# Kernel tuning notes

Measured on AMD Instinct MI355X. Metric: run time of the kernel, lower is better.

The kernel has to match this reference:

```python
import jax, jax.numpy as jnp
import numpy as np

N, A, B, C = 256, 1024, 64, 16


def setup_inputs() -> dict:
    key = jax.random.key(0)
    k1, k2, k3 = jax.random.split(key, 3)
    x = jax.random.normal(k1, (N, A), dtype=jnp.float32)
    weight = jax.random.normal(k2, (A, B * C), dtype=jnp.float32) * 0.02
    bias = jax.random.normal(k3, (B,), dtype=jnp.float32) * 0.02
    return {"x": x, "weight": weight, "bias": bias}


def reference(x, weight, bias):
    # x: [N, A]; weight: [A, B*C]; bias: [B]
    n = x.shape[0]
    mat = (x @ weight).reshape(n, B, C)              # [N, B, C]
    # pairwise L1 over the C (kernel) axis -> [N, N, B]
    l1 = jnp.abs(mat[:, None, :, :] - mat[None, :, :, :]).sum(axis=-1)
    # exp(-L1), sum over the first (broadcast) axis as in the torch code,
    # which includes the self term exp(0)=1
    out = jnp.exp(-l1).sum(axis=0) + bias            # [N, B]
    return out
```

## Files before the change

kernel.cpp:

```cpp
#include <hip/hip_runtime.h>

#define LOG2E 1.4426950408889634f

typedef __bf16 bf16x8 __attribute__((ext_vector_type(8)));
typedef float  f32x4  __attribute__((ext_vector_type(4)));

__device__ inline unsigned short f2bf(float f){
  unsigned u = __float_as_uint(f);
  unsigned r = u + 0x7FFFu + ((u >> 16) & 1u);
  return (unsigned short)(r >> 16);
}
__device__ inline unsigned pack2(float lo, float hi){
  return (unsigned)f2bf(lo) | ((unsigned)f2bf(hi) << 16);
}

__global__ __launch_bounds__(256) void k_gemm_ks(const float* __restrict__ X,
                                                 const float* __restrict__ Wm,
                                                 float* __restrict__ P){
  __shared__ unsigned short As[64 * 72];
  __shared__ unsigned short Bs[64 * 72];
  const int m0 = blockIdx.x * 64, n0 = blockIdx.y * 64;
  const int k0 = blockIdx.z * 256;
  const int t = threadIdx.x;
  const int lane = t & 63, w = t >> 6;
  const int wrow = (w & 1) * 32, wcol = (w >> 1) * 32;
  const int r16 = lane & 15, quad = lane >> 4;

  const int ar = t >> 2, aq = t & 3;
  const int bc = t & 15, bg = t >> 4;
  const float* ap = X + (size_t)(m0 + ar) * 1024 + k0 + aq * 16;
  const float* bp = Wm + (size_t)k0 * 1024 + n0 + bc * 4;

  f32x4 acc[2][2];
  #pragma unroll
  for (int p = 0; p < 2; ++p)
    #pragma unroll
    for (int q = 0; q < 2; ++q)
      #pragma unroll
      for (int e = 0; e < 4; ++e) acc[p][q][e] = 0.f;

  float4 pa[4], pb[4];
  #pragma unroll
  for (int r = 0; r < 4; ++r) pa[r] = *(const float4*)(ap + r * 4);
  #pragma unroll
  for (int r = 0; r < 4; ++r) pb[r] = *(const float4*)(bp + (size_t)(4 * bg + r) * 1024);

  #pragma unroll
  for (int kt = 0; kt < 256; kt += 64){
    __syncthreads();
    {
      unsigned short* d = &As[ar * 72 + aq * 16];
      uint4 o;
      o.x = pack2(pa[0].x, pa[0].y); o.y = pack2(pa[0].z, pa[0].w);
      o.z = pack2(pa[1].x, pa[1].y); o.w = pack2(pa[1].z, pa[1].w);
      *(uint4*)d = o;
      o.x = pack2(pa[2].x, pa[2].y); o.y = pack2(pa[2].z, pa[2].w);
      o.z = pack2(pa[3].x, pa[3].y); o.w = pack2(pa[3].z, pa[3].w);
      *(uint4*)(d + 8) = o;
    }
    {
      #pragma unroll
      for (int e = 0; e < 4; ++e){
        const int n = bc * 4 + e;
        uint2 o;
        o.x = pack2(((const float*)&pb[0])[e], ((const float*)&pb[1])[e]);
        o.y = pack2(((const float*)&pb[2])[e], ((const float*)&pb[3])[e]);
        const int cw = (bg >> 1) ^ ((n >> 3) & 7);
        *(uint2*)(&Bs[n * 72 + cw * 8 + (bg & 1) * 4]) = o;
      }
    }
    __syncthreads();
    if (kt < 192){
      #pragma unroll
      for (int r = 0; r < 4; ++r) pa[r] = *(const float4*)(ap + kt + 64 + r * 4);
      #pragma unroll
      for (int r = 0; r < 4; ++r) pb[r] = *(const float4*)(bp + (size_t)(kt + 64 + 4 * bg + r) * 1024);
    }
    #pragma unroll
    for (int kk = 0; kk < 2; ++kk){
      const int ko = kk * 32 + quad * 8;
      bf16x8 a0 = *(const bf16x8*)(&As[(wrow      + r16) * 72 + ko]);
      bf16x8 a1 = *(const bf16x8*)(&As[(wrow + 16 + r16) * 72 + ko]);
      const int c = kk * 4 + quad;
      const int nb0 = wcol + r16, nb1 = wcol + 16 + r16;
      bf16x8 b0 = *(const bf16x8*)(&Bs[nb0 * 72 + ((c ^ ((nb0 >> 3) & 7)) * 8)]);
      bf16x8 b1 = *(const bf16x8*)(&Bs[nb1 * 72 + ((c ^ ((nb1 >> 3) & 7)) * 8)]);
      acc[0][0] = __builtin_amdgcn_mfma_f32_16x16x32_bf16(a0, b0, acc[0][0], 0, 0, 0);
      acc[0][1] = __builtin_amdgcn_mfma_f32_16x16x32_bf16(a0, b1, acc[0][1], 0, 0, 0);
      acc[1][0] = __builtin_amdgcn_mfma_f32_16x16x32_bf16(a1, b0, acc[1][0], 0, 0, 0);
      acc[1][1] = __builtin_amdgcn_mfma_f32_16x16x32_bf16(a1, b1, acc[1][1], 0, 0, 0);
    }
  }
  float* Pz = P + (size_t)blockIdx.z * 64 * 256 * 16;
  #pragma unroll
  for (int p = 0; p < 2; ++p)
    #pragma unroll
    for (int q = 0; q < 2; ++q)
      #pragma unroll
      for (int r = 0; r < 4; ++r){
        const int row = m0 + wrow + p * 16 + quad * 4 + r;
        const int col = n0 + wcol + q * 16 + r16;
        Pz[(size_t)(col >> 4) * 4096 + row * 16 + (col & 15)] = acc[p][q][r];
      }
}

__global__ __launch_bounds__(1024) void k_pair(const float* __restrict__ P,
                                               const float* __restrict__ bias,
                                               float* __restrict__ out){
  __shared__ float L[256 * 20];
  __shared__ float red[16][64];
  const int b = blockIdx.x >> 2, jc = blockIdx.x & 3;
  const int t = threadIdx.x, lane = t & 63, w = t >> 6;

  {
    const int i = t >> 2, q = t & 3;
    const float* base = P + (size_t)b * 4096 + t * 4;
    float4 s0 = *(const float4*)(base);
    float4 s1 = *(const float4*)(base + 262144);
    float4 s2 = *(const float4*)(base + 524288);
    float4 s3 = *(const float4*)(base + 786432);
    float4 r;
    r.x = (s0.x + s1.x) + (s2.x + s3.x);
    r.y = (s0.y + s1.y) + (s2.y + s3.y);
    r.z = (s0.z + s1.z) + (s2.z + s3.z);
    r.w = (s0.w + s1.w) + (s2.w + s3.w);
    *(float4*)(&L[i * 20 + q * 4]) = r;
  }
  __syncthreads();

  const int j = jc * 64 + lane;
  float oj[16];
  #pragma unroll
  for (int q = 0; q < 4; ++q){
    float4 v = *(const float4*)(&L[j * 20 + q * 4]);
    oj[q*4+0] = v.x; oj[q*4+1] = v.y; oj[q*4+2] = v.z; oj[q*4+3] = v.w;
  }

  float acc = 0.f;
  const int i0 = w * 16;
  #pragma unroll 4
  for (int ii = i0; ii < i0 + 16; ++ii){
    const float4* fr = (const float4*)(&L[ii * 20]);
    float4 f0 = fr[0], f1 = fr[1], f2 = fr[2], f3 = fr[3];
    float p0 = fabsf(oj[0]  - f0.x) + fabsf(oj[1]  - f0.y)
             + fabsf(oj[2]  - f0.z) + fabsf(oj[3]  - f0.w);
    float p1 = fabsf(oj[4]  - f1.x) + fabsf(oj[5]  - f1.y)
             + fabsf(oj[6]  - f1.z) + fabsf(oj[7]  - f1.w);
    float p2 = fabsf(oj[8]  - f2.x) + fabsf(oj[9]  - f2.y)
             + fabsf(oj[10] - f2.z) + fabsf(oj[11] - f2.w);
    float p3 = fabsf(oj[12] - f3.x) + fabsf(oj[13] - f3.y)
             + fabsf(oj[14] - f3.z) + fabsf(oj[15] - f3.w);
    acc += exp2f(-LOG2E * ((p0 + p1) + (p2 + p3)));
  }
  red[w][lane] = acc;
  __syncthreads();
  if (w == 0){
    float tot = 0.f;
    #pragma unroll
    for (int ww = 0; ww < 16; ++ww) tot += red[ww][lane];
    out[(size_t)j * 64 + b] = tot + bias[b];
  }
}

extern "C" void kernel_launch(void* const* d_in, const int* in_sizes, int n_in,
                              void* d_out, int out_size, void* d_ws, size_t ws_size,
                              hipStream_t stream){
  const float* x    = (const float*)d_in[0];
  const float* W    = (const float*)d_in[1];
  const float* bias = (const float*)d_in[2];
  float* out = (float*)d_out;
  float* P   = (float*)d_ws;

  k_gemm_ks<<<dim3(4, 16, 4), 256, 0, stream>>>(x, W, P);
  k_pair<<<256, 1024, 0, stream>>>(P, bias, out);
}
```

Measured before the change: 74.12 us.

## Widen GEMM blocks to 1024 threads, loading all K-chunks at once

The split-K GEMM now runs 1024 threads per block. Four thread groups each stage one 64-wide K chunk into separate LDS buffers with a single barrier, replacing the serial 4-step K loop with its register prefetch. Each wave now computes one 16x16 output tile over all chunks instead of a 32x32 tile, using two accumulators. The bf16 conversion switches to the HIP intrinsic. The aim is more memory parallelism and fewer barriers in a latency-bound small GEMM, at the cost of 4x LDS per block and less reuse per wave.

Result: no change. 74.08 us (-0.1%).

```diff
diff --git a/kernel.cpp b/kernel.cpp
--- a/kernel.cpp
+++ b/kernel.cpp
@@ -1,43 +1,33 @@
 #include <hip/hip_runtime.h>
+#include <hip/hip_bf16.h>
 
 #define LOG2E 1.4426950408889634f
 
 typedef __bf16 bf16x8 __attribute__((ext_vector_type(8)));
 typedef float  f32x4  __attribute__((ext_vector_type(4)));
 
-__device__ inline unsigned short f2bf(float f){
-  unsigned u = __float_as_uint(f);
-  unsigned r = u + 0x7FFFu + ((u >> 16) & 1u);
-  return (unsigned short)(r >> 16);
-}
 __device__ inline unsigned pack2(float lo, float hi){
-  return (unsigned)f2bf(lo) | ((unsigned)f2bf(hi) << 16);
+  __hip_bfloat162 h = __float22bfloat162_rn(make_float2(lo, hi));
+  return *reinterpret_cast<unsigned*>(&h);
 }
 
-__global__ __launch_bounds__(256) void k_gemm_ks(const float* __restrict__ X,
-                                                 const float* __restrict__ Wm,
-                                                 float* __restrict__ P){
-  __shared__ unsigned short As[64 * 72];
-  __shared__ unsigned short Bs[64 * 72];
+__global__ __launch_bounds__(1024) void k_gemm_ks(const float* __restrict__ X,
+                                                  const float* __restrict__ Wm,
+                                                  float* __restrict__ P){
+  __shared__ unsigned short As[4][64 * 72];
+  __shared__ unsigned short Bs[4][64 * 72];
   const int m0 = blockIdx.x * 64, n0 = blockIdx.y * 64;
   const int k0 = blockIdx.z * 256;
   const int t = threadIdx.x;
   const int lane = t & 63, w = t >> 6;
-  const int wrow = (w & 1) * 32, wcol = (w >> 1) * 32;
+  const int g = t >> 8, s = t & 255;
   const int r16 = lane & 15, quad = lane >> 4;
+  const int wrow = (w & 3) * 16, wcol = (w >> 2) * 16;
 
-  const int ar = t >> 2, aq = t & 3;
-  const int bc = t & 15, bg = t >> 4;
-  const float* ap = X + (size_t)(m0 + ar) * 1024 + k0 + aq * 16;
-  const float* bp = Wm + (size_t)k0 * 1024 + n0 + bc * 4;
-
-  f32x4 acc[2][2];
-  #pragma unroll
-  for (int p = 0; p < 2; ++p)
-    #pragma unroll
-    for (int q = 0; q < 2; ++q)
-      #pragma unroll
-      for (int e = 0; e < 4; ++e) acc[p][q][e] = 0.f;
+  const int ar = s >> 2, aq = s & 3;
+  const int bc = s & 15, bg = s >> 4;
+  const float* ap = X + (size_t)(m0 + ar) * 1024 + k0 + g * 64 + aq * 16;
+  const float* bp = Wm + (size_t)(k0 + g * 64) * 1024 + n0 + bc * 4;
 
   float4 pa[4], pb[4];
   #pragma unroll
@@ -45,63 +35,49 @@
   #pragma unroll
   for (int r = 0; r < 4; ++r) pb[r] = *(const float4*)(bp + (size_t)(4 * bg + r) * 1024);
 
-  #pragma unroll
-  for (int kt = 0; kt < 256; kt += 64){
-    __syncthreads();
-    {
-      unsigned short* d = &As[ar * 72 + aq * 16];
-      uint4 o;
-      o.x = pack2(pa[0].x, pa[0].y); o.y = pack2(pa[0].z, pa[0].w);
-      o.z = pack2(pa[1].x, pa[1].y); o.w = pack2(pa[1].z, pa[1].w);
-      *(uint4*)d = o;
-      o.x = pack2(pa[2].x, pa[2].y); o.y = pack2(pa[2].z, pa[2].w);
-      o.z = pack2(pa[3].x, pa[3].y); o.w = pack2(pa[3].z, pa[3].w);
-      *(uint4*)(d + 8) = o;
-    }
-    {
-      #pragma unroll
-      for (int e = 0; e < 4; ++e){
-        const int n = bc * 4 + e;
-        uint2 o;
-        o.x = pack2(((const float*)&pb[0])[e], ((const float*)&pb[1])[e]);
-        o.y = pack2(((const float*)&pb[2])[e], ((const float*)&pb[3])[e]);
-        const int cw = (bg >> 1) ^ ((n >> 3) & 7);
-        *(uint2*)(&Bs[n * 72 + cw * 8 + (bg & 1) * 4]) = o;
-      }
-    }
-    __syncthreads();
-    if (kt < 192){
-      #pragma unroll
-      for (int r = 0; r < 4; ++r) pa[r] = *(const float4*)(ap + kt + 64 + r * 4);
-      #pragma unroll
-      for (int r = 0; r < 4; ++r) pb[r] = *(const float4*)(bp + (size_t)(kt + 64 + 4 * bg + r) * 1024);
-    }
+  {
+    unsigned short* d = &As[g][ar * 72 + aq * 16];
+    uint4 o;
+    o.x = pack2(pa[0].x, pa[0].y); o.y = pack2(pa[0].z, pa[0].w);
+    o.z = pack2(pa[1].x, pa[1].y); o.w = pack2(pa[1].z, pa[1].w);
+    *(uint4*)d = o;
+    o.x = pack2(pa[2].x, pa[2].y); o.y = pack2(pa[2].z, pa[2].w);
+    o.z = pack2(pa[3].x, pa[3].y); o.w = pack2(pa[3].z, pa[3].w);
+    *(uint4*)(d + 8) = o;
+  }
+  {
     #pragma unroll
-    for (int kk = 0; kk < 2; ++kk){
-      const int ko = kk * 32 + quad * 8;
-      bf16x8 a0 = *(const bf16x8*)(&As[(wrow      + r16) * 72 + ko]);
-      bf16x8 a1 = *(const bf16x8*)(&As[(wrow + 16 + r16) * 72 + ko]);
-      const int c = kk * 4 + quad;
-      const int nb0 = wcol + r16, nb1 = wcol + 16 + r16;
-      bf16x8 b0 = *(const bf16x8*)(&Bs[nb0 * 72 + ((c ^ ((nb0 >> 3) & 7)) * 8)]);
-      bf16x8 b1 = *(const bf16x8*)(&Bs[nb1 * 72 + ((c ^ ((nb1 >> 3) & 7)) * 8)]);
-      acc[0][0] = __builtin_amdgcn_mfma_f32_16x16x32_bf16(a0, b0, acc[0][0], 0, 0, 0);
-      acc[0][1] = __builtin_amdgcn_mfma_f32_16x16x32_bf16(a0, b1, acc[0][1], 0, 0, 0);
-      acc[1][0] = __builtin_amdgcn_mfma_f32_16x16x32_bf16(a1, b0, acc[1][0], 0, 0, 0);
-      acc[1][1] = __builtin_amdgcn_mfma_f32_16x16x32_bf16(a1, b1, acc[1][1], 0, 0, 0);
+    for (int e = 0; e < 4; ++e){
+      const int n = bc * 4 + e;
+      uint2 o;
+      o.x = pack2(((const float*)&pb[0])[e], ((const float*)&pb[1])[e]);
+      o.y = pack2(((const float*)&pb[2])[e], ((const float*)&pb[3])[e]);
+      const int cw = (bg >> 1) ^ ((n >> 3) & 7);
+      *(uint2*)(&Bs[g][n * 72 + cw * 8 + (bg & 1) * 4]) = o;
     }
   }
-  float* Pz = P + (size_t)blockIdx.z * 64 * 256 * 16;
+  __syncthreads();
+
+  f32x4 acc0, acc1;
   #pragma unroll
-  for (int p = 0; p < 2; ++p)
-    #pragma unroll
-    for (int q = 0; q < 2; ++q)
-      #pragma unroll
-      for (int r = 0; r < 4; ++r){
-        const int row = m0 + wrow + p * 16 + quad * 4 + r;
-        const int col = n0 + wcol + q * 16 + r16;
-        Pz[(size_t)(col >> 4) * 4096 + row * 16 + (col & 15)] = acc[p][q][r];
-      }
+  for (int e = 0; e < 4; ++e){ acc0[e] = 0.f; acc1[e] = 0.f; }
+  const int nn = wcol + r16;
+  const int nsw = (nn >> 3) & 7;
+  #pragma unroll
+  for (int gg = 0; gg < 4; ++gg){
+    bf16x8 a0 = *(const bf16x8*)(&As[gg][(wrow + r16) * 72 + quad * 8]);
+    bf16x8 a1 = *(const bf16x8*)(&As[gg][(wrow + r16) * 72 + 32 + quad * 8]);
+    bf16x8 b0 = *(const bf16x8*)(&Bs[gg][nn * 72 + (((quad    ) ^ nsw) * 8)]);
+    bf16x8 b1 = *(const bf16x8*)(&Bs[gg][nn * 72 + (((quad + 4) ^ nsw) * 8)]);
+    acc0 = __builtin_amdgcn_mfma_f32_16x16x32_bf16(a0, b0, acc0, 0, 0, 0);
+    acc1 = __builtin_amdgcn_mfma_f32_16x16x32_bf16(a1, b1, acc1, 0, 0, 0);
+  }
+  float* Pz = P + (size_t)blockIdx.z * 64 * 4096 + (size_t)((n0 + wcol) >> 4) * 4096;
+  #pragma unroll
+  for (int r = 0; r < 4; ++r){
+    const int row = m0 + wrow + quad * 4 + r;
+    Pz[row * 16 + r16] = acc0[r] + acc1[r];
+  }
 }
 
 __global__ __launch_bounds__(1024) void k_pair(const float* __restrict__ P,
@@ -171,6 +147,6 @@
   float* out = (float*)d_out;
   float* P   = (float*)d_ws;
 
-  k_gemm_ks<<<dim3(4, 16, 4), 256, 0, stream>>>(x, W, P);
+  k_gemm_ks<<<dim3(4, 16, 4), 1024, 0, stream>>>(x, W, P);
   k_pair<<<256, 1024, 0, stream>>>(P, bias, out);
 }
```
